# Kernel tuning notes

Measured on AMD Instinct MI355X. Metric: run time of the kernel, lower is better.

The kernel has to match this reference:

```python
import jax, jax.numpy as jnp
import numpy as np
from jax import lax

MAXV = 127.0  # 2^(8-1)-1, narrow-range int8

def _quantize_per_tensor(t):
    """Symmetric per-tensor int8 narrow-range quantization.
    Returns (int8-valued float tensor in [-127,127], scale=max_abs).
    Matches brevitas Int8*PerTensorFloat semantics used here: q = round(t*127/s),
    dequant factor applied later as out * s_x*s_w / 127^2."""
    s = jnp.max(jnp.abs(t))
    q = jnp.clip(jnp.round(t * (MAXV / s)), -MAXV, MAXV)
    return q, s

def setup_inputs() -> dict:
    key = jax.random.key(0)
    k1, k2, k3 = jax.random.split(key, 3)
    x = jax.random.normal(k1, (8, 32, 512, 512), dtype=jnp.float32)
    # kaiming-uniform-ish magnitudes
    weight = jax.random.normal(k2, (32, 32, 3, 3), dtype=jnp.float32) * 0.06
    bias = jax.random.normal(k3, (32,), dtype=jnp.float32) * 0.05
    return {"x": x, "weight": weight, "bias": bias}

def reference(x, weight, bias):
    # int8 quantize inputs & weights (per-tensor symmetric, narrow range)
    qx, sx = _quantize_per_tensor(x)
    qw, sw = _quantize_per_tensor(weight)
    # exact int8 MAC conv (reference for the approximate multiplier kernel);
    # fp32 accumulation is exact here: |sum| <= 32*9*127*127 < 2^24
    out = lax.conv_general_dilated(
        qx, qw,
        window_strides=(1, 1),
        padding=((1, 1), (1, 1)),
        dimension_numbers=("NCHW", "OIHW", "NCHW"),
    )
    # dequant: out / ((127/sx) * (127/sw)) == out * sx*sw/127^2
    out = out * (sx * sw / (MAXV * MAXV))
    return out + bias.reshape(1, -1, 1, 1)
```

## Files before the change

### kernel.cpp

```cpp
#include <hip/hip_runtime.h>
#include <hip/hip_bf16.h>


#define H 512
#define W 512
#define CIN 32
#define KOUT 32
#define NB 8
#define TH 16
#define TW 32

typedef int v4i  __attribute__((ext_vector_type(4)));
typedef int v16i __attribute__((ext_vector_type(16)));

__global__ void init_slots(unsigned* slots) {
    if (threadIdx.x < 2) slots[threadIdx.x] = 0u;
}

__device__ __forceinline__ float max4(float4 v) {
    return fmaxf(fmaxf(fabsf(v.x), fabsf(v.y)), fmaxf(fabsf(v.z), fabsf(v.w)));
}

__global__ __launch_bounds__(256)
void absmax_x(const float4* __restrict__ x, unsigned* slots, int n4) {
    const int stride = gridDim.x * blockDim.x;
    int i = blockIdx.x * blockDim.x + threadIdx.x;
    float m0 = 0.f, m1 = 0.f, m2 = 0.f, m3 = 0.f;
    for (; i + 3 * stride < n4; i += 4 * stride) {
        float4 a = x[i], b = x[i + stride], c = x[i + 2 * stride], d = x[i + 3 * stride];
        m0 = fmaxf(m0, max4(a)); m1 = fmaxf(m1, max4(b));
        m2 = fmaxf(m2, max4(c)); m3 = fmaxf(m3, max4(d));
    }
    for (; i < n4; i += stride) m0 = fmaxf(m0, max4(x[i]));
    float m = fmaxf(fmaxf(m0, m1), fmaxf(m2, m3));
    #pragma unroll
    for (int off = 32; off > 0; off >>= 1)
        m = fmaxf(m, __shfl_down(m, off));
    __shared__ float wm[4];
    int lane = threadIdx.x & 63, wid = threadIdx.x >> 6;
    if (lane == 0) wm[wid] = m;
    __syncthreads();
    if (threadIdx.x == 0) {
        m = fmaxf(fmaxf(wm[0], wm[1]), fmaxf(wm[2], wm[3]));
        atomicMax(slots, __float_as_uint(m));
    }
}

__global__ __launch_bounds__(256)
void prep_w(const float* __restrict__ w, unsigned* slots, int* __restrict__ qw) {
    float m = 0.f;
    for (int i = threadIdx.x; i < KOUT * CIN * 9; i += 256)
        m = fmaxf(m, fabsf(w[i]));
    #pragma unroll
    for (int off = 32; off > 0; off >>= 1)
        m = fmaxf(m, __shfl_down(m, off));
    __shared__ float wm[4];
    __shared__ float swsh;
    int lane = threadIdx.x & 63, wid = threadIdx.x >> 6;
    if (lane == 0) wm[wid] = m;
    __syncthreads();
    if (threadIdx.x == 0) {
        float t = fmaxf(fmaxf(wm[0], wm[1]), fmaxf(wm[2], wm[3]));
        slots[1] = __float_as_uint(t);
        swsh = t;
    }
    __syncthreads();
    const float qs = 127.f / swsh;
    for (int d = threadIdx.x; d < 9 * KOUT * 8; d += 256) {
        int tap = d >> 8, rem = d & 255, k = rem >> 3, c4 = rem & 7;
        int pk = 0;
        #pragma unroll
        for (int i = 0; i < 4; ++i) {
            int c = c4 * 4 + i;
            float q = fminf(fmaxf(rintf(w[(k * CIN + c) * 9 + tap] * qs), -127.f), 127.f);
            pk |= ((int)q & 255) << (8 * i);
        }
        qw[d] = pk;
    }
}

__global__ __launch_bounds__(256)
void conv_mfma(const float* __restrict__ x, const int* __restrict__ qw,
               const float* __restrict__ bias, const unsigned* __restrict__ slots,
               float* __restrict__ out) {
    __shared__ int lds_a[18 * 34 * 8];

    const int tid = threadIdx.x;
    const int n  = blockIdx.z;
    const int y0 = blockIdx.y * TH;
    const int x0 = blockIdx.x * TW;

    const float sx = __uint_as_float(slots[0]);
    const float sw = __uint_as_float(slots[1]);
    const float qsx = 127.f / sx;

    const float* xb = x + (size_t)n * CIN * H * W;
    for (int e = tid; e < 8 * 612; e += 256) {
        int c4  = e / 612;
        int pix = e - c4 * 612;
        int yy  = pix / 34;
        int xx  = pix - yy * 34;
        int gy = y0 + yy - 1, gx = x0 + xx - 1;
        bool ok = ((unsigned)gy < (unsigned)H) & ((unsigned)gx < (unsigned)W);
        const float* p = xb + ((size_t)(c4 * 4) * H + gy) * W + gx;
        int pk = 0;
        #pragma unroll
        for (int i = 0; i < 4; ++i) {
            float v = ok ? p[(size_t)i * H * W] : 0.f;
            int q = (int)fminf(fmaxf(rintf(v * qsx), -127.f), 127.f);
            pk |= (q & 255) << (8 * i);
        }
        lds_a[pix * 8 + c4] = pk;
    }

    const int lane = tid & 63;
    const int kcol = lane & 31;
    const int half = lane >> 5;
    const v4i* qwv = (const v4i*)qw;
    v4i wf[9];
    #pragma unroll
    for (int t = 0; t < 9; ++t)
        wf[t] = qwv[(t * KOUT + kcol) * 2 + half];

    __syncthreads();

    const int wvid  = tid >> 6;
    const int ybase = wvid * 4;
    const v4i* lap = (const v4i*)lds_a;

    v16i acc[4];
    #pragma unroll
    for (int r = 0; r < 4; ++r)
        #pragma unroll
        for (int q = 0; q < 16; ++q) acc[r][q] = 0;

    #pragma unroll
    for (int q = 0; q < 6; ++q) {
        const int ly = ybase + q;
        v4i b[3];
        #pragma unroll
        for (int dx = 0; dx < 3; ++dx)
            b[dx] = lap[(ly * 34 + kcol + dx) * 2 + half];
        #pragma unroll
        for (int dy = 0; dy < 3; ++dy) {
            const int r = q - dy;
            if (r >= 0 && r < 4) {
                #pragma unroll
                for (int dx = 0; dx < 3; ++dx)
                    acc[r] = __builtin_amdgcn_mfma_i32_32x32x32_i8(
                        wf[dy * 3 + dx], b[dx], acc[r], 0, 0, 0);
            }
        }
    }

    const float dscale = sx * sw * (1.f / 16129.f);
    float bv[16];
    #pragma unroll
    for (int reg = 0; reg < 16; ++reg)
        bv[reg] = bias[(reg & 3) + 8 * (reg >> 2) + 4 * half];

    #pragma unroll
    for (int r = 0; r < 4; ++r) {
        const int ygl = y0 + ybase + r;
        float* ob = out + (((size_t)n * KOUT * H + ygl) * W) + x0 + kcol;
        #pragma unroll
        for (int reg = 0; reg < 16; ++reg) {
            const int m = (reg & 3) + 8 * (reg >> 2) + 4 * half;
            ob[(size_t)m * H * W] = (float)acc[r][reg] * dscale + bv[reg];
        }
    }
}

extern "C" void kernel_launch(void* const* d_in, const int* in_sizes, int n_in,
                              void* d_out, int out_size, void* d_ws, size_t ws_size,
                              hipStream_t stream) {
    const float* x    = (const float*)d_in[0];
    const float* w    = (const float*)d_in[1];
    const float* bias = (const float*)d_in[2];
    float* out        = (float*)d_out;
    unsigned* slots   = (unsigned*)d_ws;
    int* qw           = (int*)((char*)d_ws + 16);

    hipLaunchKernelGGL(init_slots, dim3(1), dim3(64), 0, stream, slots);
    hipLaunchKernelGGL(absmax_x, dim3(2048), dim3(256), 0, stream,
                       (const float4*)x, slots, (NB * CIN * H * W) / 4);
    hipLaunchKernelGGL(prep_w, dim3(1), dim3(256), 0, stream, w, slots, qw);
    dim3 grid(W / TW, H / TH, NB);
    hipLaunchKernelGGL(conv_mfma, grid, dim3(256), 0, stream, x, qw, bias, slots, out);
}
```

Baseline: 579.1 us.

## Restructure conv tile load, remap blocks across XCDs, add nontemporal stores

Replaces the div/mod-heavy halo loader with a row-wise loop where each thread handles one channel group and one column, plus two tail columns per row. Block IDs are remapped so consecutive work items of the same image land on the same XCD, aiming for better L2 locality. Output stores become nontemporal to avoid polluting cache. Launch bounds now request 8 waves per SIMD-style occupancy, which may constrain registers.

```diff
diff --git a/kernel.cpp b/kernel.cpp
--- a/kernel.cpp
+++ b/kernel.cpp
@@ -9,6 +9,7 @@
 #define NB 8
 #define TH 16
 #define TW 32
+#define HW (H * W)
 
 typedef int v4i  __attribute__((ext_vector_type(4)));
 typedef int v16i __attribute__((ext_vector_type(16)));
@@ -79,38 +80,61 @@
     }
 }
 
-__global__ __launch_bounds__(256)
+__global__ __launch_bounds__(256, 8)
 void conv_mfma(const float* __restrict__ x, const int* __restrict__ qw,
                const float* __restrict__ bias, const unsigned* __restrict__ slots,
                float* __restrict__ out) {
     __shared__ int lds_a[18 * 34 * 8];
 
     const int tid = threadIdx.x;
-    const int n  = blockIdx.z;
-    const int y0 = blockIdx.y * TH;
-    const int x0 = blockIdx.x * TW;
+
+    const int id   = (int)blockIdx.x + (int)gridDim.x * ((int)blockIdx.y + (int)gridDim.y * (int)blockIdx.z);
+    const int work = (id & 7) * 512 + (id >> 3);
+    const int n    = work >> 9;
+    const int rem  = work & 511;
+    const int y0   = (rem >> 4) * TH;
+    const int x0   = (rem & 15) * TW;
 
     const float sx = __uint_as_float(slots[0]);
     const float sw = __uint_as_float(slots[1]);
     const float qsx = 127.f / sx;
 
-    const float* xb = x + (size_t)n * CIN * H * W;
-    for (int e = tid; e < 8 * 612; e += 256) {
-        int c4  = e / 612;
-        int pix = e - c4 * 612;
-        int yy  = pix / 34;
-        int xx  = pix - yy * 34;
-        int gy = y0 + yy - 1, gx = x0 + xx - 1;
-        bool ok = ((unsigned)gy < (unsigned)H) & ((unsigned)gx < (unsigned)W);
-        const float* p = xb + ((size_t)(c4 * 4) * H + gy) * W + gx;
-        int pk = 0;
-        #pragma unroll
-        for (int i = 0; i < 4; ++i) {
-            float v = ok ? p[(size_t)i * H * W] : 0.f;
-            int q = (int)fminf(fmaxf(rintf(v * qsx), -127.f), 127.f);
-            pk |= (q & 255) << (8 * i);
-        }
-        lds_a[pix * 8 + c4] = pk;
+    const float* xb = x + (size_t)n * CIN * HW;
+    const int c4 = tid >> 5;
+    const int ln = tid & 31;
+    const float* pb = xb + (size_t)(c4 * 4) * HW;
+    const int gxm = x0 - 1 + ln;
+    const bool okxm = (unsigned)gxm < (unsigned)W;
+    const int gxt = x0 + 31 + ln;
+    const bool okxt = (ln < 2) & ((unsigned)gxt < (unsigned)W);
+    const bool tail = ln < 2;
+
+    for (int yy = 0; yy < 18; ++yy) {
+        const int gy = y0 - 1 + yy;
+        const bool oky = (unsigned)gy < (unsigned)H;
+        const float* rowp = pb + (size_t)gy * W;
+        {
+            const bool ok = oky & okxm;
+            int pk = 0;
+            #pragma unroll
+            for (int i = 0; i < 4; ++i) {
+                float v = ok ? rowp[gxm + i * HW] : 0.f;
+                int q = (int)fminf(fmaxf(rintf(v * qsx), -127.f), 127.f);
+                pk |= (q & 255) << (8 * i);
+            }
+            lds_a[(yy * 34 + ln) * 8 + c4] = pk;
+        }
+        if (tail) {
+            const bool ok = oky & okxt;
+            int pk = 0;
+            #pragma unroll
+            for (int i = 0; i < 4; ++i) {
+                float v = ok ? rowp[gxt + i * HW] : 0.f;
+                int q = (int)fminf(fmaxf(rintf(v * qsx), -127.f), 127.f);
+                pk |= (q & 255) << (8 * i);
+            }
+            lds_a[(yy * 34 + 32 + ln) * 8 + c4] = pk;
+        }
     }
 
     const int lane = tid & 63;
@@ -166,7 +190,8 @@
         #pragma unroll
         for (int reg = 0; reg < 16; ++reg) {
             const int m = (reg & 3) + 8 * (reg >> 2) + 4 * half;
-            ob[(size_t)m * H * W] = (float)acc[r][reg] * dscale + bv[reg];
+            __builtin_nontemporal_store((float)acc[r][reg] * dscale + bv[reg],
+                                        &ob[(size_t)m * HW]);
         }
     }
 }
```

Measured after the change: 880.0 us. 52.0% more time.
